# Kernel tuning notes

Measured on AMD Instinct MI355X. Metric: run time of the kernel, lower is better.

## Reference

```python
import jax, jax.numpy as jnp
import numpy as np
from functools import partial

B, S, V, H, NH, NKV, M, L = 2, 2048, 51200, 1536, 24, 4, 8960, 8
DH = H // NH  # 64
EPS = 1e-6


def setup_inputs() -> dict:
    key = jax.random.key(0)
    ks = jax.random.split(key, 16)
    sc = 0.02
    w = lambda k, shape: jax.random.normal(k, shape, jnp.float32) * sc
    inp = {
        "input_ids": jax.random.randint(ks[0], (B, S), 0, V),
        "attention_mask": jnp.ones((B, S), jnp.float32),
        "embed": w(ks[1], (V, H)),
        "Wq": w(ks[2], (L, H, H)),          "bq": jnp.zeros((L, H), jnp.float32),
        "Wk": w(ks[3], (L, H, NKV * DH)),   "bk": jnp.zeros((L, NKV * DH), jnp.float32),
        "Wv": w(ks[4], (L, H, NKV * DH)),   "bv": jnp.zeros((L, NKV * DH), jnp.float32),
        "Wo": w(ks[5], (L, H, H)),
        "ln1": jnp.ones((L, H), jnp.float32),
        "ln2": jnp.ones((L, H), jnp.float32),
        "Wg": w(ks[6], (L, H, M)),
        "Wu": w(ks[7], (L, H, M)),
        "Wd": w(ks[8], (L, M, H)),
        "norm_w": jnp.ones((H,), jnp.float32),
        "W1": w(ks[9], (H, H)), "b1": jnp.zeros((H,), jnp.float32),
        "W2": w(ks[10], (H, 1)), "b2": jnp.zeros((1,), jnp.float32),
    }
    inv_freq = 1.0 / (10000.0 ** (jnp.arange(0, DH, 2, dtype=jnp.float32) / DH))
    freqs = jnp.outer(jnp.arange(S, dtype=jnp.float32), inv_freq)  # [S, DH/2]
    emb = jnp.concatenate([freqs, freqs], axis=-1)                 # [S, DH]
    inp["cos"] = jnp.cos(emb)
    inp["sin"] = jnp.sin(emb)
    return inp


def _rms(x, w):
    var = jnp.mean(x.astype(jnp.float32) ** 2, axis=-1, keepdims=True)
    return w * (x * jax.lax.rsqrt(var + EPS)).astype(x.dtype)


def _rotate_half(x):
    x1, x2 = jnp.split(x, 2, axis=-1)
    return jnp.concatenate([-x2, x1], axis=-1)


def _forward(input_ids, attention_mask, embed, Wq, bq, Wk, bk, Wv, bv, Wo,
             ln1, ln2, Wg, Wu, Wd, norm_w, W1, b1, W2, b2, cos, sin):
    scale = 1.0 / np.sqrt(DH)
    b, s = input_ids.shape
    c = cos[None, :s, None, :]  # [1,S,1,DH]
    sn = sin[None, :s, None, :]
    rope = lambda t: t * c + _rotate_half(t) * sn
    mask0 = attention_mask[:, None, None, :] == 0  # [B,1,1,S]

    def block(x, p):
        wq, bq_, wk, bk_, wv, bv_, wo, ln1w, ln2w, wg, wu, wd = p
        h = _rms(x, ln1w)
        q = (h @ wq + bq_).reshape(b, s, NH, DH)
        k = (h @ wk + bk_).reshape(b, s, NKV, DH)
        v = (h @ wv + bv_).reshape(b, s, NKV, DH)
        q, k = rope(q), rope(k)
        k = jnp.repeat(k, NH // NKV, axis=2)  # GQA expand to NH heads
        v = jnp.repeat(v, NH // NKV, axis=2)
        scores = jnp.einsum('bqhd,bkhd->bhqk', q, k) * scale
        scores = jnp.where(mask0, -1e10, scores)
        probs = jax.nn.softmax(scores, axis=-1)  # dropout: eval mode (identity)
        attn = jnp.einsum('bhqk,bkhd->bqhd', probs, v).reshape(b, s, H)
        x = x + attn @ wo
        h = _rms(x, ln2w)
        x = x + (jax.nn.sigmoid(h @ wg) * (h @ wu)) @ wd
        return x, None

    x = embed[input_ids]  # [B,S,H]
    x, _ = jax.lax.scan(block, x, (Wq, bq, Wk, bk, Wv, bv, Wo, ln1, ln2, Wg, Wu, Wd))
    x = _rms(x, norm_w)
    h = jax.nn.gelu(x @ W1 + b1, approximate=False)  # torch nn.GELU default = exact
    return h @ W2 + b2  # [B,S,1]


def reference(input_ids, attention_mask, embed, Wq, bq, Wk, bk, Wv, bv, Wo,
              ln1, ln2, Wg, Wu, Wd, norm_w, W1, b1, W2, b2, cos, sin):
    return _forward(input_ids, attention_mask, embed, Wq, bq, Wk, bk, Wv, bv, Wo,
                    ln1, ln2, Wg, Wu, Wd, norm_w, W1, b1, W2, b2, cos, sin)
```

## Files before the change

kernel.cpp:

```cpp
#include <hip/hip_runtime.h>

typedef float f32x4 __attribute__((ext_vector_type(4)));
typedef short s16x8 __attribute__((ext_vector_type(8)));
typedef unsigned short u16;
typedef unsigned short u16x4 __attribute__((ext_vector_type(4)));
typedef unsigned short u16x8 __attribute__((ext_vector_type(8)));

__device__ __forceinline__ float bf2f(u16 u){ union{unsigned int i; float f;} v; v.i=((unsigned int)u)<<16; return v.f; }
__device__ __forceinline__ u16 f2bf(float f){ union{float f; unsigned int i;} v; v.f=f; return (u16)((v.i + 0x7FFFu + ((v.i>>16)&1u))>>16); }

__device__ __forceinline__ void gld16(const void* gp, void* lp){
  __builtin_amdgcn_global_load_lds((__attribute__((address_space(1))) void*)(void*)gp,
                                   (__attribute__((address_space(3))) void*)lp, 16, 0, 0);
}

__global__ __launch_bounds__(256) void k_embed(const int* __restrict__ ids, const float* __restrict__ emb, float* __restrict__ x){
  int r = blockIdx.x;
  int id = ids[r];
  const f32x4* src = (const f32x4*)(emb + (size_t)id*1536);
  f32x4* dst = (f32x4*)(x + (size_t)r*1536);
  for (int i = threadIdx.x; i < 384; i += 256) dst[i] = src[i];
}

__global__ __launch_bounds__(256) void k_rms(const float* __restrict__ x, const float* __restrict__ w, u16* __restrict__ h){
  int r = blockIdx.x, tid = threadIdx.x;
  const f32x4* xr = (const f32x4*)(x + (size_t)r*1536);
  f32x4 v0 = xr[tid];
  float ss = v0.x*v0.x + v0.y*v0.y + v0.z*v0.z + v0.w*v0.w;
  f32x4 v1 = {0,0,0,0};
  if (tid < 128){ v1 = xr[256+tid]; ss += v1.x*v1.x + v1.y*v1.y + v1.z*v1.z + v1.w*v1.w; }
  #pragma unroll
  for (int off=32; off; off>>=1) ss += __shfl_xor(ss, off, 64);
  __shared__ float red[4];
  if ((tid&63)==0) red[tid>>6] = ss;
  __syncthreads();
  float tot = red[0]+red[1]+red[2]+red[3];
  float invr = rsqrtf(tot*(1.f/1536.f) + 1e-6f);
  const f32x4* w4 = (const f32x4*)w;
  u16x4* h4 = (u16x4*)(h + (size_t)r*1536);
  {
    f32x4 wv = w4[tid];
    u16x4 o; o.x=f2bf(v0.x*invr*wv.x); o.y=f2bf(v0.y*invr*wv.y); o.z=f2bf(v0.z*invr*wv.z); o.w=f2bf(v0.w*invr*wv.w);
    h4[tid] = o;
  }
  if (tid < 128){
    f32x4 wv = w4[256+tid];
    u16x4 o; o.x=f2bf(v1.x*invr*wv.x); o.y=f2bf(v1.y*invr*wv.y); o.z=f2bf(v1.z*invr*wv.z); o.w=f2bf(v1.w*invr*wv.w);
    h4[256+tid] = o;
  }
}

__global__ __launch_bounds__(256) void k_rms_add(float* __restrict__ x, const float* __restrict__ P, const float* __restrict__ w, u16* __restrict__ h){
  int r = blockIdx.x, tid = threadIdx.x;
  f32x4* xr = (f32x4*)(x + (size_t)r*1536);
  const f32x4* pr = (const f32x4*)(P + (size_t)r*1536);
  f32x4 v0 = xr[tid], p0 = pr[tid];
  v0.x+=p0.x; v0.y+=p0.y; v0.z+=p0.z; v0.w+=p0.w;
  xr[tid] = v0;
  float ss = v0.x*v0.x + v0.y*v0.y + v0.z*v0.z + v0.w*v0.w;
  f32x4 v1 = {0,0,0,0};
  if (tid < 128){
    v1 = xr[256+tid]; f32x4 p1 = pr[256+tid];
    v1.x+=p1.x; v1.y+=p1.y; v1.z+=p1.z; v1.w+=p1.w;
    xr[256+tid] = v1;
    ss += v1.x*v1.x + v1.y*v1.y + v1.z*v1.z + v1.w*v1.w;
  }
  #pragma unroll
  for (int off=32; off; off>>=1) ss += __shfl_xor(ss, off, 64);
  __shared__ float red[4];
  if ((tid&63)==0) red[tid>>6] = ss;
  __syncthreads();
  float tot = red[0]+red[1]+red[2]+red[3];
  float invr = rsqrtf(tot*(1.f/1536.f) + 1e-6f);
  const f32x4* w4 = (const f32x4*)w;
  u16x4* h4 = (u16x4*)(h + (size_t)r*1536);
  {
    f32x4 wv = w4[tid];
    u16x4 o; o.x=f2bf(v0.x*invr*wv.x); o.y=f2bf(v0.y*invr*wv.y); o.z=f2bf(v0.z*invr*wv.z); o.w=f2bf(v0.w*invr*wv.w);
    h4[tid] = o;
  }
  if (tid < 128){
    f32x4 wv = w4[256+tid];
    u16x4 o; o.x=f2bf(v1.x*invr*wv.x); o.y=f2bf(v1.y*invr*wv.y); o.z=f2bf(v1.z*invr*wv.z); o.w=f2bf(v1.w*invr*wv.w);
    h4[256+tid] = o;
  }
}

__device__ __forceinline__ void cvt_tile(const float* src, int K, int N, u16* dst, int k0, int n0, int roff, int mode){
  __shared__ float T[64*72];
  int tid = threadIdx.x;
  #pragma unroll
  for (int j=0;j<4;++j){
    int i = tid + j*256;
    int row = i>>4, nf = i&15;
    f32x4 vv = *(const f32x4*)(src + (size_t)(k0+row)*N + n0 + nf*4);
    *(f32x4*)&T[row*72 + nf*4] = vv;
  }
  __syncthreads();
  #pragma unroll
  for (int j=0;j<2;++j){
    int i = tid + j*256;
    int n = i>>3, kc = i&7;
    u16x8 o;
    #pragma unroll
    for (int m=0;m<8;++m) o[m] = f2bf(T[(kc*8+m)*72 + n]);
    int gn = n0 + n;
    int dr = (mode==0) ? (roff + gn) : (((gn>>4)<<5) + ((mode==2)?16:0) + (gn&15));
    *(u16x8*)(dst + (size_t)dr*K + k0 + kc*8) = o;
  }
}

__global__ __launch_bounds__(256) void k_cvt_layer(
  const float* __restrict__ Wq, const float* __restrict__ Wk, const float* __restrict__ Wv,
  const float* __restrict__ Wo, const float* __restrict__ Wg, const float* __restrict__ Wu,
  const float* __restrict__ Wd, u16* qkvt, u16* wot, u16* gut, u16* wdt)
{
  const float* src; int K, N; u16* dst; int roff=0, mode=0;
  switch (blockIdx.y){
    case 0: src=Wq; K=1536; N=1536; dst=qkvt; break;
    case 1: src=Wk; K=1536; N=256;  dst=qkvt; roff=1536; break;
    case 2: src=Wv; K=1536; N=256;  dst=qkvt; roff=1792; break;
    case 3: src=Wo; K=1536; N=1536; dst=wot;  break;
    case 4: src=Wg; K=1536; N=8960; dst=gut;  mode=1; break;
    case 5: src=Wu; K=1536; N=8960; dst=gut;  mode=2; break;
    default: src=Wd; K=8960; N=1536; dst=wdt; break;
  }
  int ntn = N>>6;
  int nt = (K>>6)*ntn;
  int t = blockIdx.x;
  if (t >= nt) return;
  cvt_tile(src, K, N, dst, (t/ntn)<<6, (t%ntn)<<6, roff, mode);
}

__global__ __launch_bounds__(256) void k_cvt_one(const float* __restrict__ src, u16* __restrict__ dst){
  int t = blockIdx.x;
  cvt_tile(src, 1536, 1536, dst, (t/24)<<6, (t%24)<<6, 0, 0);
}

#define MODE_QKV 0
#define MODE_WO 1
#define MODE_GATEUP 2
#define MODE_DOWN 3
#define MODE_W1 4

template<int MODE>
__global__ __launch_bounds__(256) void k_gemm(
  const u16* __restrict__ A, const u16* __restrict__ Bt, int K,
  int jobsPerXcd, int nc, int ksplit, int klen,
  const float* __restrict__ bq_, const float* __restrict__ bk_, const float* __restrict__ bv_,
  float* __restrict__ xio, float* __restrict__ Pf,
  const float* __restrict__ cosT, const float* __restrict__ sinT,
  u16* __restrict__ o0, u16* __restrict__ o1, u16* __restrict__ o2)
{
  int bid = blockIdx.x;
  int xcd = bid & 7, j = bid >> 3;
  int job = xcd*jobsPerXcd + (j >> 5);
  if (job >= nc*ksplit) return;
  int rowb = j & 31;
  int col = job / ksplit;
  int ks  = job - col*ksplit;
  int kbase = ks*klen;
  int nt = klen >> 5;

  __shared__ __align__(16) u16 As[4][4096], Bs[4][4096];
  int tid = threadIdx.x;
  int lane = tid & 63, w = tid >> 6;
  int wr = w >> 1, wc = w & 1;
  int row0 = rowb * 128, col0 = col * 128;
  int l15 = lane & 15, l4 = lane >> 4;
  f32x4 acc[4][4] = {};
  const u16* aBase = A + (size_t)row0*K;
  const u16* bBase = Bt + (size_t)col0*K;
  int rr0 = tid & 127, kb0 = tid >> 7;
  int kb1 = kb0 + 2;

  auto stage = [&](int bf, int kt){
    gld16(aBase + (size_t)rr0*K + kt + kb0*8, &As[bf][tid*8]);
    gld16(bBase + (size_t)rr0*K + kt + kb0*8, &Bs[bf][tid*8]);
    gld16(aBase + (size_t)rr0*K + kt + kb1*8, &As[bf][(256+tid)*8]);
    gld16(bBase + (size_t)rr0*K + kt + kb1*8, &Bs[bf][(256+tid)*8]);
  };
  stage(0, kbase); stage(1, kbase+32); stage(2, kbase+64);

  for (int t = 0; t < nt; ++t){
    if (t < nt-2)       asm volatile("s_waitcnt vmcnt(8)" ::: "memory");
    else if (t == nt-2) asm volatile("s_waitcnt vmcnt(4)" ::: "memory");
    else                asm volatile("s_waitcnt vmcnt(0)" ::: "memory");
    __builtin_amdgcn_s_barrier();
    __builtin_amdgcn_sched_barrier(0);
    if (t+3 < nt) stage((t+3)&3, kbase + (t+3)*32);
    const u16* Ab = As[t&3];
    const u16* Bb = Bs[t&3];
    s16x8 af[4], bf_[4];
    #pragma unroll
    for (int i=0;i<4;++i) af[i]  = *(const s16x8*)&Ab[((l4<<7) + wr*64 + i*16 + l15)*8];
    #pragma unroll
    for (int jj=0;jj<4;++jj) bf_[jj] = *(const s16x8*)&Bb[((l4<<7) + wc*64 + jj*16 + l15)*8];
    __builtin_amdgcn_s_setprio(1);
    #pragma unroll
    for (int i=0;i<4;++i)
      #pragma unroll
      for (int jj=0;jj<4;++jj)
        acc[i][jj] = __builtin_amdgcn_mfma_f32_16x16x32_bf16(af[i], bf_[jj], acc[i][jj], 0, 0, 0);
    __builtin_amdgcn_s_setprio(0);
  }

  #pragma unroll
  for (int i=0;i<4;++i)
    #pragma unroll
    for (int jj=0;jj<4;++jj)
      #pragma unroll
      for (int r=0;r<4;++r){
        int row = row0 + wr*64 + i*16 + l4*4 + r;
        int c   = col0 + wc*64 + jj*16 + l15;
        float v = acc[i][jj][r];
        if constexpr (MODE == MODE_QKV){
          int b = row >> 11, s = row & 2047;
          if (c < 1536){
            int d = c & 63, hd = c >> 6;
            float vv = v + bq_[c];
            float pv = acc[i][jj^2][r] + bq_[c^32];
            float cv = cosT[s*64+d], sv = sinT[s*64+d];
            float sgn = (d<32) ? -1.f : 1.f;
            float o = (vv*cv + sgn*pv*sv)*0.125f;
            o0[(size_t)(b*24+hd)*131072 + (size_t)(s>>6)*4096 + (d>>3)*512 + (s&63)*8 + (d&7)] = f2bf(o);
          } else if (c < 1792){
            int c2 = c - 1536, d = c2 & 63, kv = c2 >> 6;
            float vv = v + bk_[c2];
            float pv = acc[i][jj^2][r] + bk_[c2^32];
            float cv = cosT[s*64+d], sv = sinT[s*64+d];
            float sgn = (d<32) ? -1.f : 1.f;
            float o = vv*cv + sgn*pv*sv;
            o1[(size_t)(b*4+kv)*131072 + (size_t)(s>>6)*4096 + (d>>3)*512 + (s&63)*8 + (d&7)] = f2bf(o);
          } else {
            int c2 = c - 1792, d = c2 & 63, kv = c2 >> 6;
            float vv = v + bv_[c2];
            o2[(size_t)(b*4+kv)*131072 + (size_t)(s>>3)*512 + d*8 + (s&7)] = f2bf(vv);
          }
        } else if constexpr (MODE == MODE_WO){
          xio[(size_t)row*1536 + c] += v;
        } else if constexpr (MODE == MODE_W1){
          v += bq_[c];
          float ge = 0.5f * v * (1.f + erff(v * 0.70710678118f));
          o0[(size_t)row*1536 + c] = f2bf(ge);
        }
      }
}

template<int MODE>
__global__ __launch_bounds__(512,2) void k_gemm256(
  const u16* __restrict__ A, const u16* __restrict__ Bt, int K,
  int nrt, int ksplit, int klen,
  float* __restrict__ xio, float* __restrict__ Pf, u16* __restrict__ o0)
{
  int bid = blockIdx.x;
  int wgid = (bid & 7)*(gridDim.x >> 3) + (bid >> 3);
  int nj = nrt*ksplit;
  int ct = wgid / nj; int r2 = wgid - ct*nj;
  int rt = r2 / ksplit; int ks = r2 - rt*ksplit;

  __shared__ __align__(16) u16 lds[2][2][16384];
  int tid = threadIdx.x;
  int lane = tid & 63, wid = tid >> 6;
  int wm = wid >> 2, wn = wid & 3;
  int l15 = lane & 15, l4 = lane >> 4;
  int row0 = rt*256, col0 = ct*256;
  int kbase = ks*klen*64;

  const u16* aB = A  + (size_t)row0*K + kbase;
  const u16* bB = Bt + (size_t)col0*K + kbase;
  int rsub = tid >> 3;
  int gsw  = (lane & 7) ^ ((lane >> 3) & 7);

  f32x4 acc[8][4] = {};

  auto stage = [&](int bf, int ktElem){
    #pragma unroll
    for (int a_=0; a_<4; ++a_){
      gld16(aB + (size_t)(a_*64 + rsub)*K + ktElem + gsw*8, &lds[bf][0][(a_*512+tid)*8]);
      gld16(bB + (size_t)(a_*64 + rsub)*K + ktElem + gsw*8, &lds[bf][1][(a_*512+tid)*8]);
    }
  };

  stage(0, 0);
  for (int t = 0; t < klen; ++t){
    asm volatile("s_waitcnt vmcnt(0)" ::: "memory");
    __builtin_amdgcn_s_barrier();
    __builtin_amdgcn_sched_barrier(0);
    if (t+1 < klen) stage((t+1)&1, (t+1)*64);
    const u16* Ab = lds[t&1][0];
    const u16* Bb = lds[t&1][1];
    #pragma unroll
    for (int ksu=0; ksu<2; ++ksu){
      s16x8 af[8], bf_[4];
      #pragma unroll
      for (int i=0;i<8;++i){
        int r = wm*128 + i*16 + l15;
        af[i] = *(const s16x8*)&Ab[r*64 + (((ksu*4 + l4) ^ (l15&7))*8)];
      }
      #pragma unroll
      for (int j=0;j<4;++j){
        int c = wn*64 + j*16 + l15;
        bf_[j] = *(const s16x8*)&Bb[c*64 + (((ksu*4 + l4) ^ (l15&7))*8)];
      }
      __builtin_amdgcn_s_setprio(1);
      #pragma unroll
      for (int i=0;i<8;++i)
        #pragma unroll
        for (int j=0;j<4;++j)
          acc[i][j] = __builtin_amdgcn_mfma_f32_16x16x32_bf16(af[i], bf_[j], acc[i][j], 0, 0, 0);
      __builtin_amdgcn_s_setprio(0);
    }
  }

  if constexpr (MODE == MODE_GATEUP){
    #pragma unroll
    for (int i=0;i<8;++i)
      #pragma unroll
      for (int j2=0;j2<4;j2+=2)
        #pragma unroll
        for (int r=0;r<4;++r){
          int row = row0 + wm*128 + i*16 + l4*4 + r;
          int cp  = col0 + wn*64 + j2*16 + l15;
          float gv = acc[i][j2][r], uv = acc[i][j2+1][r];
          float sg = 1.f/(1.f + __expf(-gv));
          int n = ((cp>>5)<<4) + (cp&15);
          o0[(size_t)row*8960 + n] = f2bf(sg*uv);
        }
  } else {
    #pragma unroll
    for (int i=0;i<8;++i)
      #pragma unroll
      for (int j=0;j<4;++j)
        #pragma unroll
        for (int r=0;r<4;++r){
          int row = row0 + wm*128 + i*16 + l4*4 + r;
          int c   = col0 + wn*64 + j*16 + l15;
          float v = acc[i][j][r];
          if (ks == 0) Pf[(size_t)row*1536 + c] = v;
          else         xio[(size_t)row*1536 + c] += v;
        }
  }
}

#define MFIX 4.0f
__global__ __launch_bounds__(256) void k_attn(
  const u16* __restrict__ q, const u16* __restrict__ k, const u16* __restrict__ v,
  const float* __restrict__ mask, u16* __restrict__ attn)
{
  __shared__ __align__(16) u16 Qs[4096];
  __shared__ __align__(16) u16 Kd[3][4096];
  __shared__ __align__(16) u16 Vd[3][4096];
  __shared__ __align__(16) u16 Ps[4][1024];
  __shared__ u16 Msh[2048];
  int tid = threadIdx.x;
  int lane = tid & 63, w = tid >> 6;
  int qb = blockIdx.x;
  int bh = blockIdx.y;
  int b = bh / 24, hh = bh % 24, kv = hh / 6;
  int l15 = lane & 15, l4 = lane >> 4;

  const u16* qhead = q + ((size_t)(b*24 + hh))*131072 + qb*4096;
  const u16* khead = k + ((size_t)(b*4  + kv))*131072;
  const u16* vhead = v + ((size_t)(b*4  + kv))*131072;

  {
    const f32x4* m4 = (const f32x4*)(mask + b*2048);
    for (int i = tid; i < 512; i += 256){
      f32x4 mv = m4[i];
      u16x4 o;
      o.x = f2bf(mv.x==0.f ? -1e9f : 0.f);
      o.y = f2bf(mv.y==0.f ? -1e9f : 0.f);
      o.z = f2bf(mv.z==0.f ? -1e9f : 0.f);
      o.w = f2bf(mv.w==0.f ? -1e9f : 0.f);
      *(u16x4*)&Msh[i*4] = o;
    }
  }
  gld16(qhead + tid*8,       &Qs[tid*8]);
  gld16(qhead + (256+tid)*8, &Qs[(256+tid)*8]);

  auto stage = [&](int bf, int kt){
    gld16(khead + kt*4096 + tid*8,       &Kd[bf][tid*8]);
    gld16(khead + kt*4096 + (256+tid)*8, &Kd[bf][(256+tid)*8]);
    gld16(vhead + kt*4096 + tid*8,       &Vd[bf][tid*8]);
    gld16(vhead + kt*4096 + (256+tid)*8, &Vd[bf][(256+tid)*8]);
  };
  stage(0, 0);
  stage(1, 1);

  s16x8 aq0, aq1;
  f32x4 oacc[4] = {};
  float lsum[4] = {0.f,0.f,0.f,0.f};

  for (int t = 0; t < 32; ++t){
    if (t < 31) asm volatile("s_waitcnt vmcnt(4)" ::: "memory");
    else        asm volatile("s_waitcnt vmcnt(0)" ::: "memory");
    __builtin_amdgcn_s_barrier();
    __builtin_amdgcn_sched_barrier(0);
    if (t == 0){
      aq0 = *(const s16x8*)&Qs[(( l4   *64) + w*16 + l15)*8];
      aq1 = *(const s16x8*)&Qs[(((4+l4)*64) + w*16 + l15)*8];
    }
    if (t+2 < 32) stage((t+2)%3, t+2);
    const u16* Kb = Kd[t%3];
    const u16* Vb = Vd[t%3];
    f32x4 sk[4] = {};
    __builtin_amdgcn_s_setprio(1);
    #pragma unroll
    for (int kn=0; kn<4; ++kn){
      s16x8 bk0 = *(const s16x8*)&Kb[(( l4   *64) + kn*16 + l15)*8];
      s16x8 bk1 = *(const s16x8*)&Kb[(((4+l4)*64) + kn*16 + l15)*8];
      sk[kn] = __builtin_amdgcn_mfma_f32_16x16x32_bf16(aq0, bk0, sk[kn], 0,0,0);
      sk[kn] = __builtin_amdgcn_mfma_f32_16x16x32_bf16(aq1, bk1, sk[kn], 0,0,0);
    }
    __builtin_amdgcn_s_setprio(0);
    #pragma unroll
    for (int kn=0; kn<4; ++kn){
      float mb = bf2f(Msh[t*64 + kn*16 + l15]);
      int kk = kn*16 + l15;
      #pragma unroll
      for (int r=0;r<4;++r){
        float p = __expf(sk[kn][r] + mb - MFIX);
        lsum[r] += p;
        Ps[w][((kk>>3)*16 + l4*4 + r)*8 + (kk&7)] = f2bf(p);
      }
    }
    __builtin_amdgcn_s_setprio(1);
    #pragma unroll
    for (int ksu=0; ksu<2; ++ksu){
      s16x8 ap = *(const s16x8*)&Ps[w][((ksu*4+l4)*16 + l15)*8];
      #pragma unroll
      for (int dg=0; dg<4; ++dg){
        s16x8 bv = *(const s16x8*)&Vb[((ksu*4+l4)*64 + dg*16 + l15)*8];
        oacc[dg] = __builtin_amdgcn_mfma_f32_16x16x32_bf16(ap, bv, oacc[dg], 0,0,0);
      }
    }
    __builtin_amdgcn_s_setprio(0);
  }
  #pragma unroll
  for (int r=0;r<4;++r){
    float t = lsum[r];
    t += __shfl_xor(t, 1, 64); t += __shfl_xor(t, 2, 64);
    t += __shfl_xor(t, 4, 64); t += __shfl_xor(t, 8, 64);
    lsum[r] = 1.f / t;
  }
  #pragma unroll
  for (int dg=0;dg<4;++dg)
    #pragma unroll
    for (int r=0;r<4;++r){
      int token = b*2048 + qb*64 + w*16 + l4*4 + r;
      int col = hh*64 + dg*16 + l15;
      attn[(size_t)token*1536 + col] = f2bf(oacc[dg][r] * lsum[r]);
    }
}

__global__ __launch_bounds__(256) void k_gemv(const u16* __restrict__ h2, const float* __restrict__ W2, const float* __restrict__ b2, float* __restrict__ out){
  int tid = threadIdx.x, lane = tid & 63, w = tid >> 6;
  int r = blockIdx.x*4 + w;
  const u16* hr = h2 + (size_t)r*1536;
  float s = 0.f;
  #pragma unroll
  for (int i=0;i<24;++i){ int c = lane + i*64; s += bf2f(hr[c]) * W2[c]; }
  #pragma unroll
  for (int off=32; off; off>>=1) s += __shfl_xor(s, off, 64);
  if (lane == 0) out[r] = s + b2[0];
}

extern "C" void kernel_launch(void* const* d_in, const int* in_sizes, int n_in,
                              void* d_out, int out_size, void* d_ws, size_t ws_size,
                              hipStream_t stream)
{
  const int*   ids   = (const int*)d_in[0];
  const float* mask  = (const float*)d_in[1];
  const float* embed = (const float*)d_in[2];
  const float* Wq    = (const float*)d_in[3];
  const float* bq    = (const float*)d_in[4];
  const float* Wk    = (const float*)d_in[5];
  const float* bk    = (const float*)d_in[6];
  const float* Wv    = (const float*)d_in[7];
  const float* bv    = (const float*)d_in[8];
  const float* Wo    = (const float*)d_in[9];
  const float* ln1   = (const float*)d_in[10];
  const float* ln2   = (const float*)d_in[11];
  const float* Wg    = (const float*)d_in[12];
  const float* Wu    = (const float*)d_in[13];
  const float* Wd    = (const float*)d_in[14];
  const float* nw    = (const float*)d_in[15];
  const float* W1    = (const float*)d_in[16];
  const float* b1    = (const float*)d_in[17];
  const float* W2    = (const float*)d_in[18];
  const float* b2    = (const float*)d_in[19];
  const float* cosT  = (const float*)d_in[20];
  const float* sinT  = (const float*)d_in[21];

  char* ws = (char*)d_ws;
  float* x   = (float*)(ws + 0);
  u16* h     = (u16*)(ws + 25165824);
  u16* qb_   = (u16*)(ws + 37748736);
  u16* kb_   = (u16*)(ws + 50331648);
  u16* vb_   = (u16*)(ws + 52428800);
  u16* attn  = (u16*)(ws + 54525952);
  u16* g     = (u16*)(ws + 67108864);
  u16* qkvt  = (u16*)(ws + 140509184);
  u16* wot   = (u16*)(ws + 146800640);
  u16* gut   = (u16*)(ws + 151519232);
  u16* wdt   = (u16*)(ws + 206569472);
  float* Pf  = (float*)(ws + 37748736);
  (void)in_sizes; (void)n_in; (void)out_size; (void)ws_size;

  k_embed<<<4096, 256, 0, stream>>>(ids, embed, x);
  for (int l = 0; l < 8; ++l){
    k_cvt_layer<<<dim3(3360,7), 256, 0, stream>>>(
      Wq + (size_t)l*1536*1536, Wk + (size_t)l*1536*256, Wv + (size_t)l*1536*256,
      Wo + (size_t)l*1536*1536, Wg + (size_t)l*1536*8960, Wu + (size_t)l*1536*8960,
      Wd + (size_t)l*8960*1536, qkvt, wot, gut, wdt);
    if (l == 0) k_rms<<<4096, 256, 0, stream>>>(x, ln1, h);
    else        k_rms_add<<<4096, 256, 0, stream>>>(x, Pf, ln1 + l*1536, h);
    k_gemm<MODE_QKV><<<512, 256, 0, stream>>>(h, qkvt, 1536, 2, 16, 1, 1536,
        bq + l*1536, bk + l*256, bv + l*256, nullptr, nullptr, cosT, sinT, qb_, kb_, vb_);
    k_attn<<<dim3(32,48), 256, 0, stream>>>(qb_, kb_, vb_, mask, attn);
    k_gemm<MODE_WO><<<512, 256, 0, stream>>>(attn, wot, 1536, 2, 12, 1, 1536,
        nullptr, nullptr, nullptr, x, nullptr, nullptr, nullptr, nullptr, nullptr, nullptr);
    k_rms<<<4096, 256, 0, stream>>>(x, ln2 + l*1536, h);
    k_gemm256<MODE_GATEUP><<<1120, 512, 0, stream>>>(h, gut, 1536, 16, 1, 24,
        nullptr, nullptr, g);
    k_gemm256<MODE_DOWN><<<192, 512, 0, stream>>>(g, wdt, 8960, 16, 2, 70,
        x, Pf, nullptr);
  }
  k_cvt_one<<<576, 256, 0, stream>>>(W1, wot);
  k_rms_add<<<4096, 256, 0, stream>>>(x, Pf, nw, h);
  k_gemm<MODE_W1><<<512, 256, 0, stream>>>(h, wot, 1536, 2, 12, 1, 1536,
      b1, nullptr, nullptr, nullptr, nullptr, nullptr, nullptr, attn, nullptr, nullptr);
  k_gemv<<<1024, 256, 0, stream>>>(attn, W2, b2, (float*)d_out);
}
```

Measured before the change: 5.698 ms.

## Use XOR-swizzled row-major Q/K/V tiles and transposed score MFMA in attention

```diff
diff --git a/kernel.cpp b/kernel.cpp
--- a/kernel.cpp
+++ b/kernel.cpp
@@ -223,7 +223,8 @@
             float cv = cosT[s*64+d], sv = sinT[s*64+d];
             float sgn = (d<32) ? -1.f : 1.f;
             float o = (vv*cv + sgn*pv*sv)*0.125f;
-            o0[(size_t)(b*24+hd)*131072 + (size_t)(s>>6)*4096 + (d>>3)*512 + (s&63)*8 + (d&7)] = f2bf(o);
+            o0[(size_t)(b*24+hd)*131072 + (size_t)(s>>6)*4096
+               + (s&63)*64 + (((d>>3)^(s&7))<<3) + (d&7)] = f2bf(o);
           } else if (c < 1792){
             int c2 = c - 1536, d = c2 & 63, kv = c2 >> 6;
             float vv = v + bk_[c2];
@@ -231,11 +232,13 @@
             float cv = cosT[s*64+d], sv = sinT[s*64+d];
             float sgn = (d<32) ? -1.f : 1.f;
             float o = vv*cv + sgn*pv*sv;
-            o1[(size_t)(b*4+kv)*131072 + (size_t)(s>>6)*4096 + (d>>3)*512 + (s&63)*8 + (d&7)] = f2bf(o);
+            o1[(size_t)(b*4+kv)*131072 + (size_t)(s>>6)*4096
+               + (s&63)*64 + (((d>>3)^(s&7))<<3) + (d&7)] = f2bf(o);
           } else {
             int c2 = c - 1792, d = c2 & 63, kv = c2 >> 6;
             float vv = v + bv_[c2];
-            o2[(size_t)(b*4+kv)*131072 + (size_t)(s>>3)*512 + d*8 + (s&7)] = f2bf(vv);
+            o2[(size_t)(b*4+kv)*131072 + (size_t)(s>>6)*4096
+               + d*64 + ((((s>>3)&7)^(d&7))<<3) + (s&7)] = f2bf(vv);
           }
         } else if constexpr (MODE == MODE_WO){
           xio[(size_t)row*1536 + c] += v;
@@ -359,6 +362,7 @@
   int bh = blockIdx.y;
   int b = bh / 24, hh = bh % 24, kv = hh / 6;
   int l15 = lane & 15, l4 = lane >> 4;
+  int sw = l15 & 7;
 
   const u16* qhead = q + ((size_t)(b*24 + hh))*131072 + qb*4096;
   const u16* khead = k + ((size_t)(b*4  + kv))*131072;
@@ -390,7 +394,8 @@
 
   s16x8 aq0, aq1;
   f32x4 oacc[4] = {};
-  float lsum[4] = {0.f,0.f,0.f,0.f};
+  float lsum = 0.f;
+  u16* Pw = Ps[w];
 
   for (int t = 0; t < 32; ++t){
     if (t < 31) asm volatile("s_waitcnt vmcnt(4)" ::: "memory");
@@ -398,8 +403,9 @@
     __builtin_amdgcn_s_barrier();
     __builtin_amdgcn_sched_barrier(0);
     if (t == 0){
-      aq0 = *(const s16x8*)&Qs[(( l4   *64) + w*16 + l15)*8];
-      aq1 = *(const s16x8*)&Qs[(((4+l4)*64) + w*16 + l15)*8];
+      int qrow = w*16 + l15;
+      aq0 = *(const s16x8*)&Qs[qrow*64 + (( l4    ^ sw)<<3)];
+      aq1 = *(const s16x8*)&Qs[qrow*64 + (((4+l4) ^ sw)<<3)];
     }
     if (t+2 < 32) stage((t+2)%3, t+2);
     const u16* Kb = Kd[t%3];
@@ -408,49 +414,50 @@
     __builtin_amdgcn_s_setprio(1);
     #pragma unroll
     for (int kn=0; kn<4; ++kn){
-      s16x8 bk0 = *(const s16x8*)&Kb[(( l4   *64) + kn*16 + l15)*8];
-      s16x8 bk1 = *(const s16x8*)&Kb[(((4+l4)*64) + kn*16 + l15)*8];
-      sk[kn] = __builtin_amdgcn_mfma_f32_16x16x32_bf16(aq0, bk0, sk[kn], 0,0,0);
-      sk[kn] = __builtin_amdgcn_mfma_f32_16x16x32_bf16(aq1, bk1, sk[kn], 0,0,0);
+      int krow = kn*16 + l15;
+      s16x8 a0 = *(const s16x8*)&Kb[krow*64 + (( l4    ^ sw)<<3)];
+      s16x8 a1 = *(const s16x8*)&Kb[krow*64 + (((4+l4) ^ sw)<<3)];
+      sk[kn] = __builtin_amdgcn_mfma_f32_16x16x32_bf16(a0, aq0, sk[kn], 0,0,0);
+      sk[kn] = __builtin_amdgcn_mfma_f32_16x16x32_bf16(a1, aq1, sk[kn], 0,0,0);
     }
     __builtin_amdgcn_s_setprio(0);
     #pragma unroll
     for (int kn=0; kn<4; ++kn){
-      float mb = bf2f(Msh[t*64 + kn*16 + l15]);
-      int kk = kn*16 + l15;
+      u16x4 mv = *(const u16x4*)&Msh[t*64 + kn*16 + l4*4];
+      u16x4 pk;
       #pragma unroll
       for (int r=0;r<4;++r){
-        float p = __expf(sk[kn][r] + mb - MFIX);
-        lsum[r] += p;
-        Ps[w][((kk>>3)*16 + l4*4 + r)*8 + (kk&7)] = f2bf(p);
+        float p = __expf(sk[kn][r] + bf2f(mv[r]) - MFIX);
+        lsum += p;
+        pk[r] = f2bf(p);
       }
+      int g = kn*2 + (l4>>1);
+      *(u16x4*)&Pw[l15*64 + ((g ^ sw)<<3) + (l4&1)*4] = pk;
     }
     __builtin_amdgcn_s_setprio(1);
     #pragma unroll
     for (int ksu=0; ksu<2; ++ksu){
-      s16x8 ap = *(const s16x8*)&Ps[w][((ksu*4+l4)*16 + l15)*8];
+      s16x8 ap = *(const s16x8*)&Pw[l15*64 + (((ksu*4+l4) ^ sw)<<3)];
       #pragma unroll
       for (int dg=0; dg<4; ++dg){
-        s16x8 bv = *(const s16x8*)&Vb[((ksu*4+l4)*64 + dg*16 + l15)*8];
+        s16x8 bv = *(const s16x8*)&Vb[(dg*16+l15)*64 + (((ksu*4+l4) ^ sw)<<3)];
         oacc[dg] = __builtin_amdgcn_mfma_f32_16x16x32_bf16(ap, bv, oacc[dg], 0,0,0);
       }
     }
     __builtin_amdgcn_s_setprio(0);
   }
-  #pragma unroll
-  for (int r=0;r<4;++r){
-    float t = lsum[r];
-    t += __shfl_xor(t, 1, 64); t += __shfl_xor(t, 2, 64);
-    t += __shfl_xor(t, 4, 64); t += __shfl_xor(t, 8, 64);
-    lsum[r] = 1.f / t;
-  }
+  lsum += __shfl_xor(lsum, 16, 64);
+  lsum += __shfl_xor(lsum, 32, 64);
+  float invq[4];
+  #pragma unroll
+  for (int r=0;r<4;++r) invq[r] = 1.f / __shfl(lsum, l4*4 + r, 64);
   #pragma unroll
   for (int dg=0;dg<4;++dg)
     #pragma unroll
     for (int r=0;r<4;++r){
       int token = b*2048 + qb*64 + w*16 + l4*4 + r;
       int col = hh*64 + dg*16 + l15;
-      attn[(size_t)token*1536 + col] = f2bf(oacc[dg][r] * lsum[r]);
+      attn[(size_t)token*1536 + col] = f2bf(oacc[dg][r] * invq[r]);
     }
 }
 
```

Result: no change. 5.675 ms (-0.4%).
